# Kernel tuning notes

Hardware: AMD Instinct MI355X
Metric: run time of the kernel (lower is better)

Reference implementation:

```python
import jax, jax.numpy as jnp
import numpy as np

H, W = 64, 64
RADIUS = 3.0
N_JOINTS = 21


def setup_inputs() -> dict:
    key = jax.random.key(0)
    # keypoint coordinates (x, y) in [0, 64) per batch element and joint
    x = jax.random.uniform(key, (2048, N_JOINTS, 2), dtype=jnp.float32) * 64.0
    return {"x": x}


def reference(x):
    # Faithful vectorized form of make_kernel applied per (batch, joint):
    #   base[r, c] = exp(-((r - ceil(y))**2 + (c - ceil(x))**2) / radius)
    pts = jnp.ceil(x)                      # [B, J, 2], (x_pt, y_pt)
    px = pts[..., 0][..., None, None]      # [B, J, 1, 1]
    py = pts[..., 1][..., None, None]      # [B, J, 1, 1]
    r = jnp.arange(H, dtype=x.dtype)[:, None]   # [H, 1] row index
    c = jnp.arange(W, dtype=x.dtype)[None, :]   # [1, W] col index
    heat = jnp.exp(-(((r - py) ** 2) + ((c - px) ** 2)) / RADIUS)  # [B, J, H, W]
    return heat
```

## Files before the change

### kernel.cpp

```cpp
#include <hip/hip_runtime.h>
#include <math.h>


__global__ __launch_bounds__(256) void heatmap_kernel(
    const float* __restrict__ x, float* __restrict__ out) {
    const int bj = blockIdx.x;
    const int t  = threadIdx.x;

    const float px = ceilf(x[bj * 2 + 0]);
    const float py = ceilf(x[bj * 2 + 1]);

    constexpr float k = -0.48089834696298783f;

    const int c0 = (t & 15) * 4;
    const float d0 = (float)(c0 + 0) - px;
    const float d1 = (float)(c0 + 1) - px;
    const float d2 = (float)(c0 + 2) - px;
    const float d3 = (float)(c0 + 3) - px;
    const float cfx = exp2f(d0 * d0 * k);
    const float cfy = exp2f(d1 * d1 * k);
    const float cfz = exp2f(d2 * d2 * k);
    const float cfw = exp2f(d3 * d3 * k);

    float4* __restrict__ outv = (float4*)(out + (size_t)bj * 4096);
    const int baseRow = t >> 4;

#pragma unroll
    for (int j = 0; j < 4; ++j) {
        const float dr = (float)(j * 16 + baseRow) - py;
        const float rf = exp2f(dr * dr * k);
        float4 v;
        v.x = rf * cfx;
        v.y = rf * cfy;
        v.z = rf * cfz;
        v.w = rf * cfw;
        outv[j * 256 + t] = v;
    }
}

extern "C" void kernel_launch(void* const* d_in, const int* in_sizes, int n_in,
                              void* d_out, int out_size, void* d_ws, size_t ws_size,
                              hipStream_t stream) {
    const float* x = (const float*)d_in[0];
    float* out = (float*)d_out;
    const int nbj = in_sizes[0] / 2;
    heatmap_kernel<<<nbj, 256, 0, stream>>>(x, out);
}
```

Before: 680.6 us.

## Use persistent grid-stride blocks with nontemporal heatmap stores

```diff
diff --git a/kernel.cpp b/kernel.cpp
--- a/kernel.cpp
+++ b/kernel.cpp
@@ -2,39 +2,57 @@
 #include <math.h>
 
 
+typedef float f32x4 __attribute__((ext_vector_type(4)));
+
 __global__ __launch_bounds__(256) void heatmap_kernel(
-    const float* __restrict__ x, float* __restrict__ out) {
-    const int bj = blockIdx.x;
+    const float* __restrict__ x, float* __restrict__ out, int nbj) {
     const int t  = threadIdx.x;
-
-    const float px = ceilf(x[bj * 2 + 0]);
-    const float py = ceilf(x[bj * 2 + 1]);
+    const int c0 = (t & 15) * 4;
+    const int r0 = t >> 4;
 
     constexpr float k = -0.48089834696298783f;
 
-    const int c0 = (t & 15) * 4;
-    const float d0 = (float)(c0 + 0) - px;
-    const float d1 = (float)(c0 + 1) - px;
-    const float d2 = (float)(c0 + 2) - px;
-    const float d3 = (float)(c0 + 3) - px;
-    const float cfx = exp2f(d0 * d0 * k);
-    const float cfy = exp2f(d1 * d1 * k);
-    const float cfz = exp2f(d2 * d2 * k);
-    const float cfw = exp2f(d3 * d3 * k);
+    const float2* __restrict__ xx = (const float2*)x;
 
-    float4* __restrict__ outv = (float4*)(out + (size_t)bj * 4096);
-    const int baseRow = t >> 4;
+    int bj = blockIdx.x;
+    if (bj >= nbj) return;
+    float2 p = xx[bj];
+
+    while (true) {
+        const int bj_next = bj + gridDim.x;
+        const bool has_next = bj_next < nbj;
+        float2 pn = p;
+        if (has_next) pn = xx[bj_next];
+
+        const float px = ceilf(p.x);
+        const float py = ceilf(p.y);
+
+        const float d0 = (float)(c0 + 0) - px;
+        const float d1 = (float)(c0 + 1) - px;
+        const float d2 = (float)(c0 + 2) - px;
+        const float d3 = (float)(c0 + 3) - px;
+        const float cfx = exp2f(d0 * d0 * k);
+        const float cfy = exp2f(d1 * d1 * k);
+        const float cfz = exp2f(d2 * d2 * k);
+        const float cfw = exp2f(d3 * d3 * k);
+
+        f32x4* __restrict__ outv = (f32x4*)(out + (size_t)bj * 4096);
 
 #pragma unroll
-    for (int j = 0; j < 4; ++j) {
-        const float dr = (float)(j * 16 + baseRow) - py;
-        const float rf = exp2f(dr * dr * k);
-        float4 v;
-        v.x = rf * cfx;
-        v.y = rf * cfy;
-        v.z = rf * cfz;
-        v.w = rf * cfw;
-        outv[j * 256 + t] = v;
+        for (int j = 0; j < 4; ++j) {
+            const float dr = (float)(j * 16 + r0) - py;
+            const float rf = exp2f(dr * dr * k);
+            f32x4 v;
+            v.x = rf * cfx;
+            v.y = rf * cfy;
+            v.z = rf * cfz;
+            v.w = rf * cfw;
+            __builtin_nontemporal_store(v, &outv[j * 256 + t]);
+        }
+
+        if (!has_next) break;
+        bj = bj_next;
+        p = pn;
     }
 }
 
@@ -44,5 +62,6 @@
     const float* x = (const float*)d_in[0];
     float* out = (float*)d_out;
     const int nbj = in_sizes[0] / 2;
-    heatmap_kernel<<<nbj, 256, 0, stream>>>(x, out);
+    const int grid = nbj < 2048 ? nbj : 2048;
+    heatmap_kernel<<<grid, 256, 0, stream>>>(x, out, nbj);
 }
```

Measured after the change: 677.2 us. About the same (-0.5%).
